# Kernel tuning notes

Measured on AMD Instinct MI355X. Metric: run time of the kernel, lower is better.

## Reference

```python
import jax, jax.numpy as jnp
import numpy as np

V, E, D = 100000, 128, 60  # vocab, embedding_size, d_alpha
B, J, M, P = 512, 101, 50, 5120
EPS = 1e-6


def setup_inputs() -> dict:
    key = jax.random.key(0)
    ks = jax.random.split(key, 12)
    s = 0.5 / E
    inp = {
        'batch_titems': jax.random.randint(ks[0], (B, J), 0, V),
        'batch_citems': jax.random.randint(ks[1], (B, M), 0, V),
        'batch_pad_ids': jax.random.randint(ks[2], (2, P), 0, M),
        't_emb': jax.random.uniform(ks[3], (V, E), jnp.float32, -s, s),
        'c_emb': jax.random.uniform(ks[4], (V, E), jnp.float32, -s, s),
        'Ac_w': jax.random.normal(ks[5], (D, E), jnp.float32) * 0.05,
        'Ac_b': jnp.zeros((D,), jnp.float32),
        'At_w': jax.random.normal(ks[6], (D, E), jnp.float32) * 0.05,
        'At_b': jnp.zeros((D,), jnp.float32),
        'Bc_w': jax.random.normal(ks[7], (E, E), jnp.float32) * 0.05,
        'Bc_b': jnp.zeros((E,), jnp.float32),
        'R_w': jax.random.normal(ks[8], (E, E), jnp.float32) * 0.05,
        'R_b': jnp.zeros((E,), jnp.float32),
    }
    return inp


def reference(batch_titems, batch_citems, batch_pad_ids, t_emb, c_emb,
              Ac_w, Ac_b, At_w, At_b, Bc_w, Bc_b, R_w, R_b):
    v = t_emb[batch_titems]            # [B, J, E] target item vectors
    u = c_emb[batch_citems]            # [B, M, E] context item vectors
    tp = v @ At_w.T + At_b             # [B, J, D]
    cp = u @ Ac_w.T + Ac_b             # [B, M, D]
    # cosine similarity with torch eps clamp on norms
    dot = jnp.einsum('bjd,bmd->bjm', tp, cp)
    nt = jnp.maximum(jnp.linalg.norm(tp, axis=-1), EPS)  # [B, J]
    nc = jnp.maximum(jnp.linalg.norm(cp, axis=-1), EPS)  # [B, M]
    cos = dot / (nt[:, :, None] * nc[:, None, :])        # [B, J, M]
    # pad mask: (batch, context-pos) pairs masked across all J target rows
    mask = jnp.zeros((cos.shape[0], cos.shape[2]), bool)
    mask = mask.at[batch_pad_ids[0], batch_pad_ids[1]].set(True)
    scores = jnp.where(mask[:, None, :], -jnp.inf, cos)
    attn = jax.nn.softmax(scores, axis=-1)               # [B, J, M]
    bu = u @ Bc_w.T + Bc_b                               # [B, M, E]
    alpha = jnp.einsum('bjm,bme->bje', attn, bu)         # [B, J, E]
    return alpha @ R_w.T + R_b                           # [B, J, E]
```

## Files before the change

kernel.cpp:

```cpp
#include <hip/hip_runtime.h>

typedef unsigned short u16;
typedef unsigned int   u32;
typedef short bf8 __attribute__((ext_vector_type(8)));
typedef float f4  __attribute__((ext_vector_type(4)));

#define NB   512
#define NJ   101
#define NM   50
#define NE   128
#define ND   60
#define NP   5120
#define NT   512
#define EPSV 1e-6f

#define T_B    0
#define C_B    16128
#define H_B    25344
#define NT2_B  43776
#define NC2_B  44224
#define MSK_B  44480
#define ARENA  44736

__device__ __forceinline__ u16 f2bh(float f) {
    return (u16)((__float_as_uint(f) + 0x8000u) >> 16);
}
__device__ __forceinline__ u32 pk2(float a, float b) {
    u32 ia = __float_as_uint(a) + 0x8000u;
    u32 ib = __float_as_uint(b) + 0x8000u;
    return (ia >> 16) | (ib & 0xFFFF0000u);
}
__device__ __forceinline__ bf8 gfrag(const float* p) {
    const float4* q = (const float4*)p;
    float4 x = q[0], y = q[1];
    union { u32 u[4]; bf8 v; } r;
    r.u[0] = pk2(x.x, x.y); r.u[1] = pk2(x.z, x.w);
    r.u[2] = pk2(y.x, y.y); r.u[3] = pk2(y.z, y.w);
    return r.v;
}

__global__ __launch_bounds__(128) void w2_kernel(
    const float* __restrict__ Bc_w, const float* __restrict__ Bc_b,
    const float* __restrict__ R_w,  const float* __restrict__ R_b,
    u16* __restrict__ w2t, float* __restrict__ rb2)
{
    const int e = blockIdx.x, k = threadIdx.x;
    const float* Rrow = R_w + e * NE;
    float a0 = 0.f, a1 = 0.f, a2 = 0.f, a3 = 0.f;
    #pragma unroll 8
    for (int j = 0; j < NE; j += 4) {
        a0 += Rrow[j]     * Bc_w[j * NE + k];
        a1 += Rrow[j + 1] * Bc_w[(j + 1) * NE + k];
        a2 += Rrow[j + 2] * Bc_w[(j + 2) * NE + k];
        a3 += Rrow[j + 3] * Bc_w[(j + 3) * NE + k];
    }
    w2t[e * NE + k] = f2bh((a0 + a1) + (a2 + a3));
    float c = Bc_b[k] * Rrow[k];
    for (int o = 32; o; o >>= 1) c += __shfl_xor(c, o, 64);
    __shared__ float part[2];
    if ((k & 63) == 0) part[k >> 6] = c;
    __syncthreads();
    if (k == 0) rb2[e] = part[0] + part[1] + R_b[e];
}

__global__ __launch_bounds__(NT, 4) void aitv_kernel(
    const int* __restrict__ titems, const int* __restrict__ citems,
    const int* __restrict__ pad_ids,
    const float* __restrict__ t_emb, const float* __restrict__ c_emb,
    const float* __restrict__ Ac_w,  const float* __restrict__ Ac_b,
    const float* __restrict__ At_w,  const float* __restrict__ At_b,
    const u16* __restrict__ w2t,     const float* __restrict__ rb2g,
    float* __restrict__ out)
{
    const int b    = blockIdx.x;
    const int t    = threadIdx.x;
    const int wid  = t >> 6;
    const int lane = t & 63;
    const int l15  = lane & 15;
    const int quad = lane >> 4;

    __shared__ __align__(16) char arena[ARENA];
    u16*   tp16 = (u16*)(arena + T_B);   u16* at16 = (u16*)(arena + T_B);
    u16*   cp16 = (u16*)(arena + C_B);
    u16*   hT16 = (u16*)(arena + H_B);
    float* nt2  = (float*)(arena + NT2_B);
    float* nc2  = (float*)(arena + NC2_B);
    int*   msk  = (int*)(arena + MSK_B);

    if (t < 112) nt2[t] = 0.f;
    else if (t < 176) nc2[t - 112] = 0.f;
    else if (t < 240) msk[t - 176] = 0;
    __syncthreads();

    for (int i = t; i < NP; i += NT)
        if (pad_ids[i] == b) msk[pad_ids[NP + i]] = 1;

    for (int g = wid; g < 15; g += 8) {
        if (g < 7) {
            const int jt = g;
            const int j  = jt * 16 + l15;
            const float* vrow = t_emb + (size_t)titems[b * NJ + ((j < NJ) ? j : NJ - 1)] * NE;
            bf8 A[4];
            #pragma unroll
            for (int ks = 0; ks < 4; ks++) A[ks] = gfrag(vrow + ks * 32 + quad * 8);
            #pragma unroll
            for (int dt = 0; dt < 4; dt++) {
                const int d = dt * 16 + l15;
                const float* arow = At_w + (size_t)((d < ND) ? d : 0) * NE;
                float bv = (d < ND) ? At_b[d] : 0.f;
                f4 acc = {bv, bv, bv, bv};
                #pragma unroll
                for (int ks = 0; ks < 4; ks++)
                    acc = __builtin_amdgcn_mfma_f32_16x16x32_bf16(
                        A[ks], gfrag(arow + ks * 32 + quad * 8), acc, 0, 0, 0);
                const int j0 = jt * 16 + quad * 4;
                #pragma unroll
                for (int r = 0; r < 4; r++) {
                    float v = acc[r];
                    tp16[(j0 + r) * 72 + d] = (d < ND) ? f2bh(v) : (u16)0;
                    float q = (d < ND) ? v * v : 0.f;
                    q += __shfl_xor(q, 1, 64); q += __shfl_xor(q, 2, 64);
                    q += __shfl_xor(q, 4, 64); q += __shfl_xor(q, 8, 64);
                    if (l15 == 0) atomicAdd(&nt2[j0 + r], q);
                }
            }
        } else if (g < 11) {
            const int mt = g - 7;
            const int m  = mt * 16 + l15;
            const float* urow = c_emb + (size_t)citems[b * NM + ((m < NM) ? m : 0)] * NE;
            bf8 U[4];
            #pragma unroll
            for (int ks = 0; ks < 4; ks++) U[ks] = gfrag(urow + ks * 32 + quad * 8);
            #pragma unroll
            for (int dt = 0; dt < 4; dt++) {
                const int d = dt * 16 + l15;
                const float* arow = Ac_w + (size_t)((d < ND) ? d : 0) * NE;
                float bv = (d < ND) ? Ac_b[d] : 0.f;
                f4 acc = {bv, bv, bv, bv};
                #pragma unroll
                for (int ks = 0; ks < 4; ks++)
                    acc = __builtin_amdgcn_mfma_f32_16x16x32_bf16(
                        U[ks], gfrag(arow + ks * 32 + quad * 8), acc, 0, 0, 0);
                const int m0 = mt * 16 + quad * 4;
                #pragma unroll
                for (int r = 0; r < 4; r++) {
                    float v = acc[r];
                    cp16[(m0 + r) * 72 + d] = (d < ND) ? f2bh(v) : (u16)0;
                    float q = (d < ND) ? v * v : 0.f;
                    q += __shfl_xor(q, 1, 64); q += __shfl_xor(q, 2, 64);
                    q += __shfl_xor(q, 4, 64); q += __shfl_xor(q, 8, 64);
                    if (l15 == 0) atomicAdd(&nc2[m0 + r], q);
                }
            }
            #pragma unroll
            for (int et = 0; et < 4; et++) {
                const u16* wrow = w2t + (size_t)(et * 16 + l15) * NE;
                f4 acc = {0.f, 0.f, 0.f, 0.f};
                #pragma unroll
                for (int ks = 0; ks < 4; ks++)
                    acc = __builtin_amdgcn_mfma_f32_16x16x32_bf16(
                        *(const bf8*)(wrow + ks * 32 + quad * 8), U[ks], acc, 0, 0, 0);
                const int e0 = et * 16 + quad * 4;
                for (int r = 0; r < 4; r++)
                    hT16[(e0 + r) * 72 + mt * 16 + l15] = f2bh(acc[r]);
            }
        } else {
            const int mt = g - 11;
            const int m  = mt * 16 + l15;
            const float* urow = c_emb + (size_t)citems[b * NM + ((m < NM) ? m : 0)] * NE;
            bf8 U[4];
            #pragma unroll
            for (int ks = 0; ks < 4; ks++) U[ks] = gfrag(urow + ks * 32 + quad * 8);
            #pragma unroll
            for (int et = 4; et < 8; et++) {
                const u16* wrow = w2t + (size_t)(et * 16 + l15) * NE;
                f4 acc = {0.f, 0.f, 0.f, 0.f};
                #pragma unroll
                for (int ks = 0; ks < 4; ks++)
                    acc = __builtin_amdgcn_mfma_f32_16x16x32_bf16(
                        *(const bf8*)(wrow + ks * 32 + quad * 8), U[ks], acc, 0, 0, 0);
                const int e0 = et * 16 + quad * 4;
                for (int r = 0; r < 4; r++)
                    hT16[(e0 + r) * 72 + mt * 16 + l15] = f2bh(acc[r]);
            }
        }
    }
    __syncthreads();

    if (wid < 7) {
        const int jt = wid;
        f4 S[4];
        #pragma unroll
        for (int mt = 0; mt < 4; mt++) {
            f4 acc = {0.f, 0.f, 0.f, 0.f};
            #pragma unroll
            for (int ks = 0; ks < 2; ks++) {
                bf8 a  = *(const bf8*)(tp16 + (jt * 16 + l15) * 72 + ks * 32 + quad * 8);
                bf8 bb = *(const bf8*)(cp16 + (mt * 16 + l15) * 72 + ks * 32 + quad * 8);
                acc = __builtin_amdgcn_mfma_f32_16x16x32_bf16(a, bb, acc, 0, 0, 0);
            }
            S[mt] = acc;
        }
        bool valid[4]; float ncS[4];
        #pragma unroll
        for (int mt = 0; mt < 4; mt++) {
            int m = mt * 16 + l15;
            valid[mt] = (m < NM) && (msk[m] == 0);
            ncS[mt]   = valid[mt] ? fmaxf(sqrtf(nc2[m]), EPSV) : 1.f;
        }
        #pragma unroll
        for (int r = 0; r < 4; r++) {
            int j = jt * 16 + quad * 4 + r;
            float ntj = fmaxf(sqrtf(nt2[j]), EPSV);
            float x[4], mx = -INFINITY;
            #pragma unroll
            for (int mt = 0; mt < 4; mt++) {
                x[mt] = valid[mt] ? S[mt][r] / (ntj * ncS[mt]) : -INFINITY;
                mx = fmaxf(mx, x[mt]);
            }
            mx = fmaxf(mx, __shfl_xor(mx, 1, 64)); mx = fmaxf(mx, __shfl_xor(mx, 2, 64));
            mx = fmaxf(mx, __shfl_xor(mx, 4, 64)); mx = fmaxf(mx, __shfl_xor(mx, 8, 64));
            float p[4], sm = 0.f;
            #pragma unroll
            for (int mt = 0; mt < 4; mt++) {
                p[mt] = valid[mt] ? __expf(x[mt] - mx) : 0.f;
                sm += p[mt];
            }
            sm += __shfl_xor(sm, 1, 64); sm += __shfl_xor(sm, 2, 64);
            sm += __shfl_xor(sm, 4, 64); sm += __shfl_xor(sm, 8, 64);
            float inv = (sm > 0.f) ? 1.f / sm : 0.f;
            #pragma unroll
            for (int mt = 0; mt < 4; mt++)
                at16[j * 72 + mt * 16 + l15] = f2bh(p[mt] * inv);
        }
    }
    __syncthreads();

    for (int u = wid; u < 56; u += 8) {
        int jt = u >> 3, et = u & 7;
        float bv = rb2g[et * 16 + l15];
        f4 acc = {bv, bv, bv, bv};
        #pragma unroll
        for (int ks = 0; ks < 2; ks++) {
            bf8 a  = *(const bf8*)(at16 + (jt * 16 + l15) * 72 + ks * 32 + quad * 8);
            bf8 bb = *(const bf8*)(hT16 + (et * 16 + l15) * 72 + ks * 32 + quad * 8);
            acc = __builtin_amdgcn_mfma_f32_16x16x32_bf16(a, bb, acc, 0, 0, 0);
        }
        int e = et * 16 + l15, j0 = jt * 16 + quad * 4;
        for (int r = 0; r < 4; r++) {
            int j = j0 + r;
            if (j < NJ) out[((size_t)b * NJ + j) * NE + e] = acc[r];
        }
    }
}

extern "C" void kernel_launch(void* const* d_in, const int* in_sizes, int n_in,
                              void* d_out, int out_size, void* d_ws, size_t ws_size,
                              hipStream_t stream) {
    const int*   titems  = (const int*)d_in[0];
    const int*   citems  = (const int*)d_in[1];
    const int*   pad_ids = (const int*)d_in[2];
    const float* t_emb   = (const float*)d_in[3];
    const float* c_emb   = (const float*)d_in[4];
    const float* Ac_w    = (const float*)d_in[5];
    const float* Ac_b    = (const float*)d_in[6];
    const float* At_w    = (const float*)d_in[7];
    const float* At_b    = (const float*)d_in[8];
    const float* Bc_w    = (const float*)d_in[9];
    const float* Bc_b    = (const float*)d_in[10];
    const float* R_w     = (const float*)d_in[11];
    const float* R_b     = (const float*)d_in[12];
    float* out = (float*)d_out;

    u16*   w2t = (u16*)d_ws;
    float* rb2 = (float*)((char*)d_ws + 32768);

    w2_kernel<<<NE, NE, 0, stream>>>(Bc_w, Bc_b, R_w, R_b, w2t, rb2);
    aitv_kernel<<<NB, NT, 0, stream>>>(titems, citems, pad_ids, t_emb, c_emb,
                                       Ac_w, Ac_b, At_w, At_b, w2t, rb2, out);
}
```

Before: 184.7 us.

## Stage context embeddings in LDS once and spread the hT GEMM over all waves

Context item embedding rows are now gathered cooperatively into shared memory as bf16, once per block, instead of being re-gathered from global memory by several wave groups. The hT = Bc·u product is then split into 32 tiles handled by all 8 waves after the first barrier, rather than loaded onto waves 7-14 in the phase-1 loop. This is meant to cut redundant global gathers and even out per-wave work. In exchange, LDS use rises from about 44KB to about 62KB per block, which may lower occupancy at 4 blocks per CU.

```diff
diff --git a/kernel.cpp b/kernel.cpp
--- a/kernel.cpp
+++ b/kernel.cpp
@@ -14,13 +14,14 @@
 #define NT   512
 #define EPSV 1e-6f
 
-#define T_B    0
-#define C_B    16128
-#define H_B    25344
-#define NT2_B  43776
-#define NC2_B  44224
-#define MSK_B  44480
-#define ARENA  44736
+#define U_B    0
+#define T_B    17408
+#define C_B    33536
+#define H_B    42752
+#define NT2_B  61184
+#define NC2_B  61632
+#define MSK_B  61888
+#define ARENA  62144
 
 __device__ __forceinline__ u16 f2bh(float f) {
     return (u16)((__float_as_uint(f) + 0x8000u) >> 16);
@@ -80,6 +81,7 @@
     const int quad = lane >> 4;
 
     __shared__ __align__(16) char arena[ARENA];
+    u16*   us16 = (u16*)(arena + U_B);   u32* us32 = (u32*)(arena + U_B);
     u16*   tp16 = (u16*)(arena + T_B);   u16* at16 = (u16*)(arena + T_B);
     u16*   cp16 = (u16*)(arena + C_B);
     u16*   hT16 = (u16*)(arena + H_B);
@@ -87,6 +89,16 @@
     float* nc2  = (float*)(arena + NC2_B);
     int*   msk  = (int*)(arena + MSK_B);
 
+    for (int i = t; i < 64 * 64; i += NT) {
+        int row = i >> 6, c2 = i & 63;
+        u32 val = 0;
+        if (row < NM) {
+            int idx = citems[b * NM + row];
+            float2 x = *(const float2*)(c_emb + (size_t)idx * NE + 2 * c2);
+            val = pk2(x.x, x.y);
+        }
+        us32[row * 68 + c2] = val;
+    }
     if (t < 112) nt2[t] = 0.f;
     else if (t < 176) nc2[t - 112] = 0.f;
     else if (t < 240) msk[t - 176] = 0;
@@ -95,7 +107,7 @@
     for (int i = t; i < NP; i += NT)
         if (pad_ids[i] == b) msk[pad_ids[NP + i]] = 1;
 
-    for (int g = wid; g < 15; g += 8) {
+    for (int g = wid; g < 11; g += 8) {
         if (g < 7) {
             const int jt = g;
             const int j  = jt * 16 + l15;
@@ -124,13 +136,12 @@
                     if (l15 == 0) atomicAdd(&nt2[j0 + r], q);
                 }
             }
-        } else if (g < 11) {
+        } else {
             const int mt = g - 7;
-            const int m  = mt * 16 + l15;
-            const float* urow = c_emb + (size_t)citems[b * NM + ((m < NM) ? m : 0)] * NE;
             bf8 U[4];
             #pragma unroll
-            for (int ks = 0; ks < 4; ks++) U[ks] = gfrag(urow + ks * 32 + quad * 8);
+            for (int ks = 0; ks < 4; ks++)
+                U[ks] = *(const bf8*)(us16 + (mt * 16 + l15) * 136 + ks * 32 + quad * 8);
             #pragma unroll
             for (int dt = 0; dt < 4; dt++) {
                 const int d = dt * 16 + l15;
@@ -152,41 +163,26 @@
                     if (l15 == 0) atomicAdd(&nc2[m0 + r], q);
                 }
             }
-            #pragma unroll
-            for (int et = 0; et < 4; et++) {
-                const u16* wrow = w2t + (size_t)(et * 16 + l15) * NE;
-                f4 acc = {0.f, 0.f, 0.f, 0.f};
-                #pragma unroll
-                for (int ks = 0; ks < 4; ks++)
-                    acc = __builtin_amdgcn_mfma_f32_16x16x32_bf16(
-                        *(const bf8*)(wrow + ks * 32 + quad * 8), U[ks], acc, 0, 0, 0);
-                const int e0 = et * 16 + quad * 4;
-                for (int r = 0; r < 4; r++)
-                    hT16[(e0 + r) * 72 + mt * 16 + l15] = f2bh(acc[r]);
-            }
-        } else {
-            const int mt = g - 11;
-            const int m  = mt * 16 + l15;
-            const float* urow = c_emb + (size_t)citems[b * NM + ((m < NM) ? m : 0)] * NE;
-            bf8 U[4];
-            #pragma unroll
-            for (int ks = 0; ks < 4; ks++) U[ks] = gfrag(urow + ks * 32 + quad * 8);
-            #pragma unroll
-            for (int et = 4; et < 8; et++) {
-                const u16* wrow = w2t + (size_t)(et * 16 + l15) * NE;
-                f4 acc = {0.f, 0.f, 0.f, 0.f};
-                #pragma unroll
-                for (int ks = 0; ks < 4; ks++)
-                    acc = __builtin_amdgcn_mfma_f32_16x16x32_bf16(
-                        *(const bf8*)(wrow + ks * 32 + quad * 8), U[ks], acc, 0, 0, 0);
-                const int e0 = et * 16 + quad * 4;
-                for (int r = 0; r < 4; r++)
-                    hT16[(e0 + r) * 72 + mt * 16 + l15] = f2bh(acc[r]);
-            }
-        }
-    }
-    __syncthreads();
-
+        }
+    }
+    __syncthreads();
+
+    for (int u = wid; u < 32; u += 8) {
+        int et = u >> 2, mt = u & 3;
+        const u16* wrow = w2t + (size_t)(et * 16 + l15) * NE;
+        bf8 U[4];
+        #pragma unroll
+        for (int ks = 0; ks < 4; ks++)
+            U[ks] = *(const bf8*)(us16 + (mt * 16 + l15) * 136 + ks * 32 + quad * 8);
+        f4 acc = {0.f, 0.f, 0.f, 0.f};
+        #pragma unroll
+        for (int ks = 0; ks < 4; ks++)
+            acc = __builtin_amdgcn_mfma_f32_16x16x32_bf16(
+                *(const bf8*)(wrow + ks * 32 + quad * 8), U[ks], acc, 0, 0, 0);
+        const int e0 = et * 16 + quad * 4;
+        for (int r = 0; r < 4; r++)
+            hT16[(e0 + r) * 72 + mt * 16 + l15] = f2bh(acc[r]);
+    }
     if (wid < 7) {
         const int jt = wid;
         f4 S[4];
```

New measurement: 182.6 us. Within noise of the previous version (-1.2%).
